# Kernel tuning notes

Measured on AMD Instinct MI355X. Metric: run time of the kernel, lower is better.

Reference implementation:

```python
import jax, jax.numpy as jnp
import numpy as np
import math

# B queries, N complex ambient dim, M codebook entries, S payload dim, K quad nodes
B, N, M, S, K = 1024, 128, 8192, 256, 8
EPS_TOTAL = 1e-3
OVERLAP, ANISO = 0.25, 0.75
_t, _w = np.polynomial.hermite.hermgauss(K)
GH_T = jnp.asarray(_t, jnp.float32)
GH_W = jnp.asarray(_w, jnp.float32)


def _init_sigmas():
    # mirrors CPSFFusedCodebook._init_sigmas (log-space for numerical safety at N=128)
    rho = 1.0 + ANISO
    logV = (N / 2.0) * math.log(math.pi) - math.lgamma(N / 2.0 + 1.0)
    log_r = (math.log(OVERLAP) - math.log(M) - logV - math.log(rho)) / N
    r_perp = math.exp(log_r)
    s_perp = 2.0 * math.pi * r_perp ** 2
    return rho * rho * s_perp, s_perp


def setup_inputs() -> dict:
    key = jax.random.key(0)
    ks = jax.random.split(key, 12)
    u = lambda k, sh: jax.random.uniform(k, sh, jnp.float32, -1.0, 1.0)
    s_par, s_perp = _init_sigmas()
    return {
        "z_re": u(ks[0], (B, N)), "z_im": u(ks[1], (B, N)),
        "d_re": u(ks[2], (B, N)), "d_im": u(ks[3], (B, N)),
        "zj_re": 0.5 * u(ks[4], (M, N)), "zj_im": 0.5 * u(ks[5], (M, N)),
        "dj_re": 0.5 * u(ks[6], (M, N)), "dj_im": 0.5 * u(ks[7], (M, N)),
        "T_re": u(ks[8], (M, S)), "T_im": u(ks[9], (M, S)),
        "alpha": jax.random.uniform(ks[10], (M,), jnp.float32, 0.5, 1.5),
        "sigma_par": jnp.full((M,), s_par, jnp.float32),
        "sigma_perp": jnp.full((M,), s_perp, jnp.float32),
    }


def _unit(xr, xi):
    n = jnp.sqrt(jnp.sum(xr * xr + xi * xi, -1, keepdims=True))
    n = jnp.where(n == 0, jnp.ones_like(n), n)
    return xr / n, xi / n


def _forward(z_re, z_im, d_re, d_im, zj_re, zj_im, dj_re, dj_im,
             T_re, T_im, alpha, sigma_par, sigma_perp):
    tiny = jnp.float32(np.finfo(np.float32).tiny)
    dur, dui = _unit(d_re, d_im)          # autonorm_vec_d
    djr, dji = _unit(dj_re, dj_im)        # autonorm_vec_d_j
    a = jnp.maximum(alpha, tiny)
    sp = jnp.maximum(sigma_par, tiny)
    sq = jnp.maximum(sigma_perp, tiny)

    # proj[b,m] = <d_j, z - z_j> (conj-linear in d_j); all via GEMMs, no [B,M,N] tensor
    pr = z_re @ djr.T + z_im @ dji.T - jnp.sum(djr * zj_re + dji * zj_im, -1)[None, :]
    pi = z_im @ djr.T - z_re @ dji.T - jnp.sum(djr * zj_im - dji * zj_re, -1)[None, :]

    # |z - z_j|^2 via GEMM expansion
    dz2 = (jnp.sum(z_re * z_re + z_im * z_im, -1)[:, None]
           + jnp.sum(zj_re * zj_re + zj_im * zj_im, -1)[None, :]
           - 2.0 * (z_re @ zj_re.T + z_im @ zj_im.T))
    perp2 = jnp.maximum(dz2 - (pr * pr + pi * pi), 0.0)  # component orthogonal to d_j

    # Gauss-Hermite quadrature along the codebook direction, scaled per-code
    scale = jnp.sqrt(sp / jnp.pi)                     # [M]
    t = GH_T[None, :] * scale[:, None]                # [M,K] quad offsets
    par2 = (pr[:, :, None] - t[None]) ** 2 + (pi * pi)[:, :, None]   # [B,M,K]
    env = jnp.exp(-jnp.pi * (par2 / sp[None, :, None]
                             + (perp2 / sq[None, :])[:, :, None]))
    rho = jnp.einsum('bmk,k->bm', env, GH_W) * (scale / jnp.sqrt(jnp.pi))[None, :]

    # angular alignment |<d_j, d>|^2
    ar = dur @ djr.T + dui @ dji.T
    ai = dui @ djr.T - dur @ dji.T
    align = ar * ar + ai * ai

    w = a[None, :] * align * rho                      # [B,M] real mixture weights
    den = jnp.sum(w, -1) + EPS_TOTAL                  # [B]
    out_re = (w @ T_re) / den[:, None]                # [B,S]
    out_im = (w @ T_im) / den[:, None]
    return jnp.stack([out_re, out_im], -1)            # [B,S,2] == complex [B,S]


def reference(z_re, z_im, d_re, d_im, zj_re, zj_im, dj_re, dj_im,
              T_re, T_im, alpha, sigma_par, sigma_perp):
    return _forward(z_re, z_im, d_re, d_im, zj_re, zj_im, dj_re, dj_im,
                    T_re, T_im, alpha, sigma_par, sigma_perp)
```

## Files before the change

kernel.cpp:

```cpp
#include <hip/hip_runtime.h>
#include <math.h>

#define Bq 1024
#define Nn 128
#define Mm 8192
#define Ss 256

typedef _Float16 f16;
typedef _Float16 f16x8 __attribute__((ext_vector_type(8)));
typedef float f32x4 __attribute__((ext_vector_type(4)));

#define PI_F 3.14159265358979323846f
#define INV_SQRT_PI 0.5641895835477563f
#define TINY_F 1.17549435e-38f
#define EPS_TOTAL 1e-3f
#define WSC 1024.0f

#define GLOAD16(g, l) \
    __builtin_amdgcn_global_load_lds((const __attribute__((address_space(1))) void*)(g), \
                                     (__attribute__((address_space(3))) void*)(l), 16, 0, 0)

__global__ void cpsf_prep_a(const float* __restrict__ z_re, const float* __restrict__ z_im,
                            const float* __restrict__ d_re, const float* __restrict__ d_im,
                            float* __restrict__ z2, f16* __restrict__ Az, f16* __restrict__ Au)
{
    const int b = blockIdx.x * 4 + (threadIdx.x >> 6);
    const int l = threadIdx.x & 63;
    const int o = b * Nn;
    float dr0 = d_re[o + l], dr1 = d_re[o + l + 64];
    float di0 = d_im[o + l], di1 = d_im[o + l + 64];
    float zr0 = z_re[o + l], zr1 = z_re[o + l + 64];
    float zi0 = z_im[o + l], zi1 = z_im[o + l + 64];
    float sd = dr0*dr0 + di0*di0 + dr1*dr1 + di1*di1;
    float sz = zr0*zr0 + zi0*zi0 + zr1*zr1 + zi1*zi1;
#pragma unroll
    for (int off = 1; off < 64; off <<= 1) {
        sd += __shfl_xor(sd, off);
        sz += __shfl_xor(sz, off);
    }
    float nd = sqrtf(sd);
    nd = (nd == 0.0f) ? 1.0f : nd;
    float inv = 1.0f / nd;
    if (l == 0) z2[b] = sz;
    const int o2 = b * 256;
    Az[o2 + l]       = (f16)zr0;  Az[o2 + 64 + l]  = (f16)zr1;
    Az[o2 + 128 + l] = (f16)zi0;  Az[o2 + 192 + l] = (f16)zi1;
    Au[o2 + l]       = (f16)(dr0*inv);  Au[o2 + 64 + l]  = (f16)(dr1*inv);
    Au[o2 + 128 + l] = (f16)(di0*inv);  Au[o2 + 192 + l] = (f16)(di1*inv);
}

__global__ void cpsf_prep_m(const float* __restrict__ zj_re, const float* __restrict__ zj_im,
                            const float* __restrict__ dj_re, const float* __restrict__ dj_im,
                            const float* __restrict__ alpha, const float* __restrict__ sp_,
                            const float* __restrict__ sq_, float* __restrict__ cm,
                            f16* __restrict__ Bp)
{
    const int m = blockIdx.x * 4 + (threadIdx.x >> 6);
    const int l = threadIdx.x & 63;
    const int o = m * Nn;
    float dr0 = dj_re[o + l], dr1 = dj_re[o + l + 64];
    float di0 = dj_im[o + l], di1 = dj_im[o + l + 64];
    float zr0 = zj_re[o + l], zr1 = zj_re[o + l + 64];
    float zi0 = zj_im[o + l], zi1 = zj_im[o + l + 64];
    float snd = dr0*dr0 + di0*di0 + dr1*dr1 + di1*di1;
    float sc1 = dr0*zr0 + di0*zi0 + dr1*zr1 + di1*zi1;
    float sc2 = dr0*zi0 - di0*zr0 + dr1*zi1 - di1*zr1;
    float sz2 = zr0*zr0 + zi0*zi0 + zr1*zr1 + zi1*zi1;
#pragma unroll
    for (int off = 1; off < 64; off <<= 1) {
        snd += __shfl_xor(snd, off);
        sc1 += __shfl_xor(sc1, off);
        sc2 += __shfl_xor(sc2, off);
        sz2 += __shfl_xor(sz2, off);
    }
    float nd = sqrtf(snd);
    nd = (nd == 0.0f) ? 1.0f : nd;
    float inv = 1.0f / nd;
    const size_t b0o = (size_t)m * 256;
    const size_t b1o = ((size_t)Mm + m) * 256;
    const size_t b2o = ((size_t)2 * Mm + m) * 256;
    Bp[b0o + l]       = (f16)(dr0*inv);  Bp[b0o + 64 + l]  = (f16)(dr1*inv);
    Bp[b0o + 128 + l] = (f16)(di0*inv);  Bp[b0o + 192 + l] = (f16)(di1*inv);
    Bp[b1o + l]       = (f16)(-di0*inv); Bp[b1o + 64 + l]  = (f16)(-di1*inv);
    Bp[b1o + 128 + l] = (f16)(dr0*inv);  Bp[b1o + 192 + l] = (f16)(dr1*inv);
    Bp[b2o + l]       = (f16)zr0;        Bp[b2o + 64 + l]  = (f16)zr1;
    Bp[b2o + 128 + l] = (f16)zi0;        Bp[b2o + 192 + l] = (f16)zi1;
    if (l == 0) {
        cm[1*Mm + m] = sc1 * inv;
        cm[2*Mm + m] = sc2 * inv;
        cm[3*Mm + m] = sz2;
        float sp = fmaxf(sp_[m], TINY_F);
        float sq = fmaxf(sq_[m], TINY_F);
        float sc = sqrtf(sp / PI_F);
        cm[4*Mm + m] = PI_F / sp;
        cm[5*Mm + m] = PI_F / sq;
        cm[6*Mm + m] = fmaxf(alpha[m], TINY_F) * sc * INV_SQRT_PI;
        cm[7*Mm + m] = sc;
    }
}

__global__ void cpsf_pack_tt(const float* __restrict__ T_re, const float* __restrict__ T_im,
                             f16* __restrict__ Tt)
{
    __shared__ float tr[64][65], ti[64][65];
    const int mb = blockIdx.x * 64, sb = blockIdx.y * 64;
    const int tid = threadIdx.x;
    const int i0 = tid >> 6, j = tid & 63;
#pragma unroll
    for (int it = 0; it < 16; ++it) {
        int i = it * 4 + i0;
        tr[i][j] = T_re[(size_t)(mb + i) * Ss + sb + j];
        ti[i][j] = T_im[(size_t)(mb + i) * Ss + sb + j];
    }
    __syncthreads();
#pragma unroll
    for (int it = 0; it < 16; ++it) {
        int jj = it * 4 + i0;
        int sp = (sb + jj) * 2;
        Tt[(size_t)sp * Mm + mb + j]       = (f16)tr[j][jj];
        Tt[(size_t)(sp + 1) * Mm + mb + j] = (f16)ti[j][jj];
    }
}

__global__ __launch_bounds__(256, 3) void cpsf_gemm_w(
    const f16* __restrict__ Az, const f16* __restrict__ Au,
    const f16* __restrict__ Bp, const float* __restrict__ cm,
    const float* __restrict__ z2v, f16* __restrict__ wbuf,
    float* __restrict__ den)
{
    __shared__ __align__(16) f16 sm[2560 * 8];

    const int tid = threadIdx.x;
    const int wid = tid >> 6;
    const int lane = tid & 63;
    const int q = lane >> 4;
    const int li = lane & 15;
    const int mb0 = blockIdx.x * 64;
    const int bb0 = blockIdx.y * 64;
    const int wb0 = (wid >> 1) * 32;
    const int wm0 = (wid & 1) * 32;

    const f16* gp[10];
    f16* lb[10];
#pragma unroll
    for (int i = 0; i < 10; ++i) {
        int c = i * 4 + wid;
        const f16* src;
        if (c < 8) {
            src = Az + (size_t)(bb0 + lane) * 256 + c * 8;
        } else if (c < 16) {
            int g = c - 8;
            src = Au + (size_t)(bb0 + lane) * 256 + g * 8;
        } else {
            int c2 = c - 16, g = c2 / 3, p = c2 % 3;
            src = Bp + ((size_t)p * Mm + mb0 + lane) * 256 + g * 8;
        }
        gp[i] = src;
        lb[i] = sm + (size_t)c * 64 * 8;
    }

    f32x4 accP[2][2][3];
    f32x4 accQ[2][2][2];
#pragma unroll
    for (int t = 0; t < 2; ++t)
#pragma unroll
        for (int u = 0; u < 2; ++u) {
#pragma unroll
            for (int p = 0; p < 3; ++p) accP[t][u][p] = (f32x4){0.f,0.f,0.f,0.f};
#pragma unroll
            for (int p = 0; p < 2; ++p) accQ[t][u][p] = (f32x4){0.f,0.f,0.f,0.f};
        }

    for (int ks = 0; ks < 4; ++ks) {
        __syncthreads();
#pragma unroll
        for (int i = 0; i < 10; ++i) {
            GLOAD16(gp[i], lb[i]);
            gp[i] += 64;
        }
        __syncthreads();
#pragma unroll
        for (int j = 0; j < 2; ++j) {
            const int g = j * 4 + q;
            f16x8 az[2], au[2], bf[3][2];
#pragma unroll
            for (int t = 0; t < 2; ++t) {
                az[t] = *(const f16x8*)(sm + (size_t)(g * 64 + wb0 + t * 16 + li) * 8);
                au[t] = *(const f16x8*)(sm + (size_t)(512 + g * 64 + wb0 + t * 16 + li) * 8);
            }
#pragma unroll
            for (int p = 0; p < 3; ++p)
#pragma unroll
                for (int u = 0; u < 2; ++u)
                    bf[p][u] = *(const f16x8*)(sm + (size_t)(1024 + (g * 3 + p) * 64 + wm0 + u * 16 + li) * 8);
#pragma unroll
            for (int t = 0; t < 2; ++t)
#pragma unroll
                for (int u = 0; u < 2; ++u) {
#pragma unroll
                    for (int p = 0; p < 3; ++p)
                        accP[t][u][p] = __builtin_amdgcn_mfma_f32_16x16x32_f16(az[t], bf[p][u], accP[t][u][p], 0, 0, 0);
                    accQ[t][u][0] = __builtin_amdgcn_mfma_f32_16x16x32_f16(au[t], bf[0][u], accQ[t][u][0], 0, 0, 0);
                    accQ[t][u][1] = __builtin_amdgcn_mfma_f32_16x16x32_f16(au[t], bf[1][u], accQ[t][u][1], 0, 0, 0);
                }
        }
    }

    const float GT[8] = {-2.9306374202572440f, -1.9816567566958429f,
                         -1.1571937124467802f, -0.3811869902073221f,
                          0.3811869902073221f,  1.1571937124467802f,
                          1.9816567566958429f,  2.9306374202572440f};
    const float GW[8] = {1.9960407221136762e-04f, 1.7077983007413475e-02f,
                         2.0780232581489188e-01f, 6.6114701255824129e-01f,
                         6.6114701255824129e-01f, 2.0780232581489188e-01f,
                         1.7077983007413475e-02f, 1.9960407221136762e-04f};

    float c1[2], c2[2], zj2[2], isp[2], isq[2], cf[2], scl[2];
#pragma unroll
    for (int u = 0; u < 2; ++u) {
        int mg = mb0 + wm0 + u * 16 + li;
        c1[u]  = cm[1*Mm + mg];  c2[u]  = cm[2*Mm + mg];
        zj2[u] = cm[3*Mm + mg];  isp[u] = cm[4*Mm + mg];
        isq[u] = cm[5*Mm + mg];  cf[u]  = cm[6*Mm + mg];
        scl[u] = cm[7*Mm + mg];
    }

    float dsum[2][4];
#pragma unroll
    for (int t = 0; t < 2; ++t)
#pragma unroll
        for (int r = 0; r < 4; ++r) dsum[t][r] = 0.f;

#pragma unroll
    for (int t = 0; t < 2; ++t) {
#pragma unroll
        for (int r = 0; r < 4; ++r) {
            const int b = bb0 + wb0 + t * 16 + q * 4 + r;
            const float z2b = z2v[b];
#pragma unroll
            for (int u = 0; u < 2; ++u) {
                float pr = accP[t][u][0][r] - c1[u];
                float pi = accP[t][u][1][r] - c2[u];
                float dz2 = z2b + zj2[u] - 2.0f * accP[t][u][2][r];
                float perp2 = fmaxf(dz2 - pr * pr - pi * pi, 0.0f);
                float base = -(isq[u] * perp2 + isp[u] * pi * pi);
                float rho = 0.0f;
#pragma unroll
                for (int k = 0; k < 8; ++k) {
                    float dd = pr - scl[u] * GT[k];
                    rho = fmaf(GW[k], __expf(base - isp[u] * dd * dd), rho);
                }
                float ar = accQ[t][u][0][r], ai = accQ[t][u][1][r];
                float wv = cf[u] * (ar * ar + ai * ai) * rho;
                dsum[t][r] += wv;
                wbuf[(size_t)b * Mm + mb0 + wm0 + u * 16 + li] = (f16)(wv * WSC);
            }
        }
    }
#pragma unroll
    for (int t = 0; t < 2; ++t)
#pragma unroll
        for (int r = 0; r < 4; ++r) {
            float v = dsum[t][r];
            v += __shfl_xor(v, 1);
            v += __shfl_xor(v, 2);
            v += __shfl_xor(v, 4);
            v += __shfl_xor(v, 8);
            if (li == 0) atomicAdd(den + bb0 + wb0 + t * 16 + q * 4 + r, v);
        }
}

__global__ __launch_bounds__(256, 4) void cpsf_gemm_out(
    const f16* __restrict__ wbuf, const f16* __restrict__ Tt,
    float* __restrict__ oacc)
{
    __shared__ __align__(16) f16 sm[1536 * 8];
    const int tid = threadIdx.x;
    const int wid = tid >> 6;
    const int lane = tid & 63;
    const int q = lane >> 4;
    const int li = lane & 15;
    const int sb0 = blockIdx.x * 128;
    const int bb0 = blockIdx.y * 64;
    const int kz0 = blockIdx.z * 1024;
    const int wb0 = (wid >> 1) * 32;
    const int ws0 = (wid & 1) * 64;

    const f16* gp[6];
    f16* lb[6];
#pragma unroll
    for (int i = 0; i < 6; ++i) {
        int c = i * 4 + wid;
        const f16* src;
        f16* dst;
        if (c < 8) {
            src = wbuf + (size_t)(bb0 + lane) * Mm + kz0 + c * 8;
            dst = sm + (size_t)c * 64 * 8;
        } else {
            int c2 = c - 8, g = c2 >> 1, rh = c2 & 1;
            src = Tt + (size_t)(sb0 + rh * 64 + lane) * Mm + kz0 + g * 8;
            dst = sm + (size_t)(512 + g * 128 + rh * 64) * 8;
        }
        gp[i] = src;
        lb[i] = dst;
    }

    f32x4 acc[2][4];
#pragma unroll
    for (int t = 0; t < 2; ++t)
#pragma unroll
        for (int u = 0; u < 4; ++u) acc[t][u] = (f32x4){0.f,0.f,0.f,0.f};

    for (int ks = 0; ks < 16; ++ks) {
        __syncthreads();
#pragma unroll
        for (int i = 0; i < 6; ++i) {
            GLOAD16(gp[i], lb[i]);
            gp[i] += 64;
        }
        __syncthreads();
#pragma unroll
        for (int j = 0; j < 2; ++j) {
            const int g = j * 4 + q;
            f16x8 af[2], bf[4];
#pragma unroll
            for (int t = 0; t < 2; ++t)
                af[t] = *(const f16x8*)(sm + (size_t)(g * 64 + wb0 + t * 16 + li) * 8);
#pragma unroll
            for (int u = 0; u < 4; ++u)
                bf[u] = *(const f16x8*)(sm + (size_t)(512 + g * 128 + ws0 + u * 16 + li) * 8);
#pragma unroll
            for (int t = 0; t < 2; ++t)
#pragma unroll
                for (int u = 0; u < 4; ++u)
                    acc[t][u] = __builtin_amdgcn_mfma_f32_16x16x32_f16(af[t], bf[u], acc[t][u], 0, 0, 0);
        }
    }
#pragma unroll
    for (int t = 0; t < 2; ++t)
#pragma unroll
        for (int u = 0; u < 4; ++u)
#pragma unroll
            for (int r = 0; r < 4; ++r)
                atomicAdd(oacc + (size_t)(bb0 + wb0 + t * 16 + q * 4 + r) * 512 + sb0 + ws0 + u * 16 + li,
                          acc[t][u][r]);
}

__global__ void cpsf_fin(const float* __restrict__ oacc, const float* __restrict__ den,
                         float* __restrict__ out)
{
    int i = blockIdx.x * 256 + threadIdx.x;
    float d = (den[i >> 9] + EPS_TOTAL) * WSC;
    out[i] = oacc[i] / d;
}

extern "C" void kernel_launch(void* const* d_in, const int* in_sizes, int n_in,
                              void* d_out, int out_size, void* d_ws, size_t ws_size,
                              hipStream_t stream)
{
    (void)in_sizes; (void)n_in; (void)out_size; (void)ws_size;
    const float* z_re  = (const float*)d_in[0];
    const float* z_im  = (const float*)d_in[1];
    const float* d_re  = (const float*)d_in[2];
    const float* d_im  = (const float*)d_in[3];
    const float* zj_re = (const float*)d_in[4];
    const float* zj_im = (const float*)d_in[5];
    const float* dj_re = (const float*)d_in[6];
    const float* dj_im = (const float*)d_in[7];
    const float* T_re  = (const float*)d_in[8];
    const float* T_im  = (const float*)d_in[9];
    const float* alpha = (const float*)d_in[10];
    const float* s_par = (const float*)d_in[11];
    const float* s_perp= (const float*)d_in[12];

    char* w8 = (char*)d_ws;
    const size_t o_out = 0;
    const size_t o_den = o_out + (size_t)Bq * 512 * 4;
    const size_t o_z2  = o_den + 4096;
    const size_t o_cm  = o_z2 + 4096;
    const size_t o_az  = o_cm + (size_t)8 * Mm * 4;
    const size_t o_au  = o_az + (size_t)Bq * 256 * 2;
    const size_t o_bp  = o_au + (size_t)Bq * 256 * 2;
    const size_t o_tt  = o_bp + (size_t)3 * Mm * 256 * 2;
    const size_t o_wb  = o_tt + (size_t)512 * Mm * 2;

    float* oacc = (float*)(w8 + o_out);
    float* den  = (float*)(w8 + o_den);
    float* z2   = (float*)(w8 + o_z2);
    float* cm   = (float*)(w8 + o_cm);
    f16*   Az   = (f16*)(w8 + o_az);
    f16*   Au   = (f16*)(w8 + o_au);
    f16*   Bp   = (f16*)(w8 + o_bp);
    f16*   Tt   = (f16*)(w8 + o_tt);
    f16*   wb   = (f16*)(w8 + o_wb);

    hipMemsetAsync(d_ws, 0, o_cm, stream);

    cpsf_prep_a<<<Bq / 4, 256, 0, stream>>>(z_re, z_im, d_re, d_im, z2, Az, Au);
    cpsf_prep_m<<<Mm / 4, 256, 0, stream>>>(zj_re, zj_im, dj_re, dj_im,
                                            alpha, s_par, s_perp, cm, Bp);
    cpsf_pack_tt<<<dim3(Mm / 64, Ss / 64), 256, 0, stream>>>(T_re, T_im, Tt);
    cpsf_gemm_w<<<dim3(Mm / 64, Bq / 64), 256, 0, stream>>>(Az, Au, Bp, cm, z2, wb, den);
    cpsf_gemm_out<<<dim3(4, Bq / 64, Mm / 1024), 256, 0, stream>>>(wb, Tt, oacc);
    cpsf_fin<<<(Bq * 512) / 256, 256, 0, stream>>>(oacc, den, (float*)d_out);
}
```

Baseline: 253.9 us.

## Rewrite weight GEMM as single-wave 32x32 tiles with double-buffered LDS loads

```diff
diff --git a/kernel.cpp b/kernel.cpp
--- a/kernel.cpp
+++ b/kernel.cpp
@@ -9,6 +9,7 @@
 typedef _Float16 f16;
 typedef _Float16 f16x8 __attribute__((ext_vector_type(8)));
 typedef float f32x4 __attribute__((ext_vector_type(4)));
+typedef float f32x16 __attribute__((ext_vector_type(16)));
 
 #define PI_F 3.14159265358979323846f
 #define INV_SQRT_PI 0.5641895835477563f
@@ -122,89 +123,58 @@
     }
 }
 
-__global__ __launch_bounds__(256, 3) void cpsf_gemm_w(
+__global__ __launch_bounds__(64, 3) void cpsf_gemm_w(
     const f16* __restrict__ Az, const f16* __restrict__ Au,
     const f16* __restrict__ Bp, const float* __restrict__ cm,
     const float* __restrict__ z2v, f16* __restrict__ wbuf,
     float* __restrict__ den)
 {
-    __shared__ __align__(16) f16 sm[2560 * 8];
-
-    const int tid = threadIdx.x;
-    const int wid = tid >> 6;
-    const int lane = tid & 63;
-    const int q = lane >> 4;
-    const int li = lane & 15;
-    const int mb0 = blockIdx.x * 64;
-    const int bb0 = blockIdx.y * 64;
-    const int wb0 = (wid >> 1) * 32;
-    const int wm0 = (wid & 1) * 32;
-
-    const f16* gp[10];
-    f16* lb[10];
-#pragma unroll
-    for (int i = 0; i < 10; ++i) {
-        int c = i * 4 + wid;
-        const f16* src;
-        if (c < 8) {
-            src = Az + (size_t)(bb0 + lane) * 256 + c * 8;
-        } else if (c < 16) {
-            int g = c - 8;
-            src = Au + (size_t)(bb0 + lane) * 256 + g * 8;
+    __shared__ __align__(16) f16 sm[5120];
+
+    const int lane = threadIdx.x;
+    const int mb0 = blockIdx.x * 32;
+    const int bb0 = blockIdx.y * 32;
+
+    const int srow = lane >> 1;
+    const int sh   = (lane & 1) * 8;
+    const f16* g0 = Az + (size_t)(bb0 + srow) * 256 + sh;
+    const f16* g1 = Au + (size_t)(bb0 + srow) * 256 + sh;
+    const f16* g2 = Bp + (size_t)(mb0 + srow) * 256 + sh;
+    const f16* g3 = g2 + (size_t)Mm * 256;
+    const f16* g4 = g3 + (size_t)Mm * 256;
+
+    f32x16 aP0 = {}, aP1 = {}, aP2 = {}, aQ0 = {}, aQ1 = {};
+
+#define ISSUE(buf) { \
+    GLOAD16(g0, sm + (buf)*2560 +    0); g0 += 16; \
+    GLOAD16(g1, sm + (buf)*2560 +  512); g1 += 16; \
+    GLOAD16(g2, sm + (buf)*2560 + 1024); g2 += 16; \
+    GLOAD16(g3, sm + (buf)*2560 + 1536); g3 += 16; \
+    GLOAD16(g4, sm + (buf)*2560 + 2048); g4 += 16; }
+
+    ISSUE(0)
+    const int fo = (lane & 31) * 16 + (lane >> 5) * 8;
+#pragma unroll
+    for (int ks = 0; ks < 16; ++ks) {
+        if (ks < 15) {
+            ISSUE((ks + 1) & 1)
+            __builtin_amdgcn_s_waitcnt(0x0F75);
         } else {
-            int c2 = c - 16, g = c2 / 3, p = c2 % 3;
-            src = Bp + ((size_t)p * Mm + mb0 + lane) * 256 + g * 8;
-        }
-        gp[i] = src;
-        lb[i] = sm + (size_t)c * 64 * 8;
-    }
-
-    f32x4 accP[2][2][3];
-    f32x4 accQ[2][2][2];
-#pragma unroll
-    for (int t = 0; t < 2; ++t)
-#pragma unroll
-        for (int u = 0; u < 2; ++u) {
-#pragma unroll
-            for (int p = 0; p < 3; ++p) accP[t][u][p] = (f32x4){0.f,0.f,0.f,0.f};
-#pragma unroll
-            for (int p = 0; p < 2; ++p) accQ[t][u][p] = (f32x4){0.f,0.f,0.f,0.f};
-        }
-
-    for (int ks = 0; ks < 4; ++ks) {
-        __syncthreads();
-#pragma unroll
-        for (int i = 0; i < 10; ++i) {
-            GLOAD16(gp[i], lb[i]);
-            gp[i] += 64;
-        }
-        __syncthreads();
-#pragma unroll
-        for (int j = 0; j < 2; ++j) {
-            const int g = j * 4 + q;
-            f16x8 az[2], au[2], bf[3][2];
-#pragma unroll
-            for (int t = 0; t < 2; ++t) {
-                az[t] = *(const f16x8*)(sm + (size_t)(g * 64 + wb0 + t * 16 + li) * 8);
-                au[t] = *(const f16x8*)(sm + (size_t)(512 + g * 64 + wb0 + t * 16 + li) * 8);
-            }
-#pragma unroll
-            for (int p = 0; p < 3; ++p)
-#pragma unroll
-                for (int u = 0; u < 2; ++u)
-                    bf[p][u] = *(const f16x8*)(sm + (size_t)(1024 + (g * 3 + p) * 64 + wm0 + u * 16 + li) * 8);
-#pragma unroll
-            for (int t = 0; t < 2; ++t)
-#pragma unroll
-                for (int u = 0; u < 2; ++u) {
-#pragma unroll
-                    for (int p = 0; p < 3; ++p)
-                        accP[t][u][p] = __builtin_amdgcn_mfma_f32_16x16x32_f16(az[t], bf[p][u], accP[t][u][p], 0, 0, 0);
-                    accQ[t][u][0] = __builtin_amdgcn_mfma_f32_16x16x32_f16(au[t], bf[0][u], accQ[t][u][0], 0, 0, 0);
-                    accQ[t][u][1] = __builtin_amdgcn_mfma_f32_16x16x32_f16(au[t], bf[1][u], accQ[t][u][1], 0, 0, 0);
-                }
-        }
-    }
+            __builtin_amdgcn_s_waitcnt(0x0F70);
+        }
+        const f16* sb = sm + (ks & 1) * 2560;
+        f16x8 az = *(const f16x8*)(sb + fo);
+        f16x8 au = *(const f16x8*)(sb + 512 + fo);
+        f16x8 b0 = *(const f16x8*)(sb + 1024 + fo);
+        f16x8 b1 = *(const f16x8*)(sb + 1536 + fo);
+        f16x8 b2 = *(const f16x8*)(sb + 2048 + fo);
+        aP0 = __builtin_amdgcn_mfma_f32_32x32x16_f16(az, b0, aP0, 0, 0, 0);
+        aP1 = __builtin_amdgcn_mfma_f32_32x32x16_f16(az, b1, aP1, 0, 0, 0);
+        aP2 = __builtin_amdgcn_mfma_f32_32x32x16_f16(az, b2, aP2, 0, 0, 0);
+        aQ0 = __builtin_amdgcn_mfma_f32_32x32x16_f16(au, b0, aQ0, 0, 0, 0);
+        aQ1 = __builtin_amdgcn_mfma_f32_32x32x16_f16(au, b1, aQ1, 0, 0, 0);
+    }
+#undef ISSUE
 
     const float GT[8] = {-2.9306374202572440f, -1.9816567566958429f,
                          -1.1571937124467802f, -0.3811869902073221f,
@@ -215,59 +185,39 @@
                          6.6114701255824129e-01f, 2.0780232581489188e-01f,
                          1.7077983007413475e-02f, 1.9960407221136762e-04f};
 
-    float c1[2], c2[2], zj2[2], isp[2], isq[2], cf[2], scl[2];
-#pragma unroll
-    for (int u = 0; u < 2; ++u) {
-        int mg = mb0 + wm0 + u * 16 + li;
-        c1[u]  = cm[1*Mm + mg];  c2[u]  = cm[2*Mm + mg];
-        zj2[u] = cm[3*Mm + mg];  isp[u] = cm[4*Mm + mg];
-        isq[u] = cm[5*Mm + mg];  cf[u]  = cm[6*Mm + mg];
-        scl[u] = cm[7*Mm + mg];
-    }
-
-    float dsum[2][4];
-#pragma unroll
-    for (int t = 0; t < 2; ++t)
-#pragma unroll
-        for (int r = 0; r < 4; ++r) dsum[t][r] = 0.f;
-
-#pragma unroll
-    for (int t = 0; t < 2; ++t) {
-#pragma unroll
-        for (int r = 0; r < 4; ++r) {
-            const int b = bb0 + wb0 + t * 16 + q * 4 + r;
-            const float z2b = z2v[b];
-#pragma unroll
-            for (int u = 0; u < 2; ++u) {
-                float pr = accP[t][u][0][r] - c1[u];
-                float pi = accP[t][u][1][r] - c2[u];
-                float dz2 = z2b + zj2[u] - 2.0f * accP[t][u][2][r];
-                float perp2 = fmaxf(dz2 - pr * pr - pi * pi, 0.0f);
-                float base = -(isq[u] * perp2 + isp[u] * pi * pi);
-                float rho = 0.0f;
-#pragma unroll
-                for (int k = 0; k < 8; ++k) {
-                    float dd = pr - scl[u] * GT[k];
-                    rho = fmaf(GW[k], __expf(base - isp[u] * dd * dd), rho);
-                }
-                float ar = accQ[t][u][0][r], ai = accQ[t][u][1][r];
-                float wv = cf[u] * (ar * ar + ai * ai) * rho;
-                dsum[t][r] += wv;
-                wbuf[(size_t)b * Mm + mb0 + wm0 + u * 16 + li] = (f16)(wv * WSC);
-            }
-        }
-    }
-#pragma unroll
-    for (int t = 0; t < 2; ++t)
-#pragma unroll
-        for (int r = 0; r < 4; ++r) {
-            float v = dsum[t][r];
-            v += __shfl_xor(v, 1);
-            v += __shfl_xor(v, 2);
-            v += __shfl_xor(v, 4);
-            v += __shfl_xor(v, 8);
-            if (li == 0) atomicAdd(den + bb0 + wb0 + t * 16 + q * 4 + r, v);
-        }
+    const int m = mb0 + (lane & 31);
+    const float c1  = cm[1*Mm + m], c2  = cm[2*Mm + m];
+    const float zj2 = cm[3*Mm + m], isp = cm[4*Mm + m];
+    const float isq = cm[5*Mm + m], cf  = cm[6*Mm + m];
+    const float scl = cm[7*Mm + m];
+    const int bhalf = 4 * (lane >> 5);
+
+#pragma unroll
+    for (int reg = 0; reg < 16; ++reg) {
+        const int b = bb0 + (reg & 3) + 8 * (reg >> 2) + bhalf;
+        const float z2b = z2v[b];
+        float pr = aP0[reg] - c1;
+        float pi = aP1[reg] - c2;
+        float dz2 = z2b + zj2 - 2.0f * aP2[reg];
+        float perp2 = fmaxf(dz2 - pr * pr - pi * pi, 0.0f);
+        float base = -(isq * perp2 + isp * pi * pi);
+        float rho = 0.0f;
+#pragma unroll
+        for (int k = 0; k < 8; ++k) {
+            float dd = pr - scl * GT[k];
+            rho = fmaf(GW[k], __expf(base - isp * dd * dd), rho);
+        }
+        float ar = aQ0[reg], ai = aQ1[reg];
+        float wv = cf * (ar * ar + ai * ai) * rho;
+        wbuf[(size_t)b * Mm + m] = (f16)(wv * WSC);
+        float v = wv;
+        v += __shfl_xor(v, 1);
+        v += __shfl_xor(v, 2);
+        v += __shfl_xor(v, 4);
+        v += __shfl_xor(v, 8);
+        v += __shfl_xor(v, 16);
+        if ((lane & 31) == 0) atomicAdd(den + b, v);
+    }
 }
 
 __global__ __launch_bounds__(256, 4) void cpsf_gemm_out(
@@ -394,13 +344,13 @@
     f16*   Tt   = (f16*)(w8 + o_tt);
     f16*   wb   = (f16*)(w8 + o_wb);
 
-    hipMemsetAsync(d_ws, 0, o_cm, stream);
+    (void)hipMemsetAsync(d_ws, 0, o_cm, stream);
 
     cpsf_prep_a<<<Bq / 4, 256, 0, stream>>>(z_re, z_im, d_re, d_im, z2, Az, Au);
     cpsf_prep_m<<<Mm / 4, 256, 0, stream>>>(zj_re, zj_im, dj_re, dj_im,
                                             alpha, s_par, s_perp, cm, Bp);
     cpsf_pack_tt<<<dim3(Mm / 64, Ss / 64), 256, 0, stream>>>(T_re, T_im, Tt);
-    cpsf_gemm_w<<<dim3(Mm / 64, Bq / 64), 256, 0, stream>>>(Az, Au, Bp, cm, z2, wb, den);
+    cpsf_gemm_w<<<dim3(Mm / 32, Bq / 32), 64, 0, stream>>>(Az, Au, Bp, cm, z2, wb, den);
     cpsf_gemm_out<<<dim3(4, Bq / 64, Mm / 1024), 256, 0, stream>>>(wb, Tt, oacc);
     cpsf_fin<<<(Bq * 512) / 256, 256, 0, stream>>>(oacc, den, (float*)d_out);
 }
```

New measurement: 305.6 us. 1.2x slower.
